# Optimization experiments

Measured on AMD Instinct MI355X. Metric: run time of the kernel, lower is better.

## Reference

```python
import jax, jax.numpy as jnp
import numpy as np

# OFDM/MIMO constants from the source module
N = 512        # subcarriers
N_R = 2        # rx antennas
N_T = 2        # tx antennas
M_BITS = 4     # bits per QAM symbol (16-QAM)
CP = 7         # cyclic prefix = IsiDuration - 1
NO = 1e-5
EBNO_DB = 10.0
BATCH = 4096

# unit-average-power 16-QAM: per-axis levels, index = re_idx + 4*im_idx, bits LSB-first
LEV = jnp.asarray(np.array([-3.0, -1.0, 1.0, 3.0], np.float32) / np.sqrt(10.0))
_idx = np.arange(2 ** M_BITS)
CONST = jnp.asarray(((np.array([-3., -1., 1., 3.]) / np.sqrt(10.))[_idx % 4]
                     + 1j * (np.array([-3., -1., 1., 3.]) / np.sqrt(10.))[_idx // 4]).astype(np.complex64))


def setup_inputs() -> dict:
    key = jax.random.key(0)
    k1, k2, k3 = jax.random.split(key, 3)
    y_data_nld = jax.random.normal(k1, (BATCH, N_R, N + CP, 2), jnp.float32)
    y_ls = jax.random.normal(k2, (BATCH, N_R, N + CP, 2), jnp.float32)
    x_ls_idx = jax.random.randint(k3, (BATCH, N_T, N), 0, 2 ** M_BITS)
    return {"y_data_nld": y_data_nld, "y_ls": y_ls, "x_ls_idx": x_ls_idx}


def _c(x):
    return jax.lax.complex(x[..., 0], x[..., 1])


def _interp_c(xq, xp, fp):
    # fp: [M, P] complex -> [M, N] complex, linear interp per row (np.interp semantics)
    return jax.vmap(lambda fr, fi: jnp.interp(xq, xp, fr) + 1j * jnp.interp(xq, xp, fi))(fp.real, fp.imag)


def _forward(y_data_nld, y_ls, x_ls_idx):
    B = y_data_nld.shape[0]
    pi = 10.0 ** (EBNO_DB / 10.0) * NO * N          # = 0.0512
    sqrt_pi = jnp.sqrt(jnp.float32(pi))

    # strip CP, FFT, normalize (1/N * fft)
    Y = jnp.fft.fft(_c(y_data_nld)[..., CP:], axis=-1) / N            # [B, N_r, N]
    Y_l = jnp.fft.fft(_c(y_ls)[..., CP:], axis=-1) / (N * sqrt_pi)     # [B, N_r, N]

    x_ls = CONST[x_ls_idx]                                             # [B, N_t, N] pilots

    # comb-type LS estimates + linear interpolation to all N subcarriers
    xq = jnp.arange(N, dtype=jnp.float32)
    H_t = []
    for t in range(N_T):
        comb = jnp.arange(t, N, N_T)                                   # pilot subcarriers for tx t
        pil = Y_l[:, :, comb] / x_ls[:, None, t, comb]                 # [B, N_r, N/N_t]
        if t == 0:
            xp = jnp.concatenate([comb, jnp.array([N - 1])]).astype(jnp.float32)
            fp = jnp.concatenate([pil, pil[..., -1:]], axis=-1)
        else:
            xp = jnp.concatenate([jnp.array([0]), comb]).astype(jnp.float32)
            fp = jnp.concatenate([pil[..., :1], pil], axis=-1)
        P = fp.shape[-1]
        H_t.append(_interp_c(xq, xp, fp.reshape(B * N_R, P)).reshape(B, N_R, N))
    Hm = jnp.stack(H_t, axis=-1)                                       # [B, N_r, N, N_t]
    Hm = jnp.transpose(Hm, (0, 2, 1, 3))                               # [B, N, N_r, N_t]

    # per-subcarrier 2x2 linear solve: X_hat = H^{-1} Y / sqrt(pi)
    X_hat = jnp.linalg.solve(Hm, jnp.transpose(Y, (0, 2, 1))[..., None])[..., 0] / sqrt_pi  # [B, N, N_t]
    x_hat_ri = jnp.stack([X_hat.real, X_hat.imag], axis=-1)            # [B, N, N_t, 2]

    # nearest-QAM demap (square 16-QAM: per-axis argmin == joint argmin), bits LSB-first
    vre = jnp.argmin((X_hat.real[..., None] - LEV) ** 2, axis=-1)      # [B, N, N_t]
    vim = jnp.argmin((X_hat.imag[..., None] - LEV) ** 2, axis=-1)
    qidx = vre + 4 * vim
    bits = (qidx[..., None] >> jnp.arange(M_BITS)) & 1                 # [B, N, N_t, m]
    b_hat = jnp.transpose(bits, (0, 2, 1, 3)).reshape(B, N_T, N * M_BITS).astype(jnp.float32)
    return x_hat_ri, b_hat


def reference(y_data_nld, y_ls, x_ls_idx):
    return _forward(y_data_nld, y_ls, x_ls_idx)
```

## Files before the change

kernel.cpp:

```cpp
#include <hip/hip_runtime.h>
#include <math.h>

namespace {

constexpr int NSC  = 512;
constexpr int CP   = 7;
constexpr int NTOT = 519;

__device__ __forceinline__ int padidx(int x) { return x + (x >> 5); }

struct cf { float x, y; };
__device__ __forceinline__ cf cadd(cf a, cf b) { return {a.x + b.x, a.y + b.y}; }
__device__ __forceinline__ cf csub(cf a, cf b) { return {a.x - b.x, a.y - b.y}; }
__device__ __forceinline__ cf cmul(cf a, cf b) { return {a.x*b.x - a.y*b.y, a.x*b.y + a.y*b.x}; }
__device__ __forceinline__ cf mni(cf a) { return {a.y, -a.x}; }

__device__ __forceinline__ void fft8(cf a[8]) {
    const float s = 0.70710678118654752f;
    cf b0 = a[0], b1 = a[4], b2 = a[2], b3 = a[6];
    cf b4 = a[1], b5 = a[5], b6 = a[3], b7 = a[7];
    cf c0 = cadd(b0, b1), c1 = csub(b0, b1);
    cf c2 = cadd(b2, b3), c3 = csub(b2, b3);
    cf c4 = cadd(b4, b5), c5 = csub(b4, b5);
    cf c6 = cadd(b6, b7), c7 = csub(b6, b7);
    cf d0 = cadd(c0, c2), d2 = csub(c0, c2);
    cf d1 = cadd(c1, mni(c3)), d3 = csub(c1, mni(c3));
    cf d4 = cadd(c4, c6), d6 = csub(c4, c6);
    cf d5 = cadd(c5, mni(c7)), d7 = csub(c5, mni(c7));
    cf e5 = { s * (d5.x + d5.y), s * (d5.y - d5.x) };
    cf e6 = mni(d6);
    cf e7 = { s * (d7.y - d7.x), -s * (d7.x + d7.y) };
    a[0] = cadd(d0, d4); a[4] = csub(d0, d4);
    a[1] = cadd(d1, e5); a[5] = csub(d1, e5);
    a[2] = cadd(d2, e6); a[6] = csub(d2, e6);
    a[3] = cadd(d3, e7); a[7] = csub(d3, e7);
}

struct cd { double x, y; };
__device__ __forceinline__ cd cmuld(cd a, cd b) { return {a.x*b.x - a.y*b.y, a.x*b.y + a.y*b.x}; }
__device__ __forceinline__ cd csubd(cd a, cd b) { return {a.x - b.x, a.y - b.y}; }
__device__ __forceinline__ cd cdivd(cd a, cd b) {
    double d = b.x*b.x + b.y*b.y;
    return {(a.x*b.x + a.y*b.y) / d, (a.y*b.x - a.x*b.y) / d};
}

__global__ __launch_bounds__(256) void ofdm_mimo_kernel(
    const float* __restrict__ y_data,
    const float* __restrict__ y_ls,
    const int*   __restrict__ x_idx,
    float*       __restrict__ out,
    int B)
{
    __shared__ float sr[4][528];
    __shared__ float si[4][528];
    __shared__ float2 pil[2][2][NSC / 2];

    const int b   = blockIdx.x;
    const int tid = threadIdx.x;
    const int q   = tid >> 6;
    const int t   = tid & 63;

    const float data_scale = 1.0f / 512.0f;
    const float ls_scale   = (float)(1.0 / (512.0 * 0.22627416997969522));

    const int r = q & 1;
    const float* srcp = (q < 2) ? y_data : y_ls;
    const float sc = (q < 2) ? data_scale : ls_scale;
    const float2* xin = (const float2*)(srcp + ((size_t)(b * 2 + r) * NTOT + CP) * 2);

    cf a[8];
    #pragma unroll
    for (int n2 = 0; n2 < 8; ++n2) {
        float2 v = xin[t + 64 * n2];
        a[n2] = { v.x * sc, v.y * sc };
    }
    fft8(a);

    {
        const int n1 = t >> 3;
        const float w64 = -6.2831853071795864769f / 64.0f;
        #pragma unroll
        for (int k0 = 1; k0 < 8; ++k0) {
            float sn, cs;
            __sincosf(w64 * (float)(n1 * k0), &sn, &cs);
            a[k0] = cmul(a[k0], {cs, sn});
        }
    }
    #pragma unroll
    for (int k0 = 0; k0 < 8; ++k0) {
        int p = padidx(t * 8 + k0);
        sr[q][p] = a[k0].x;
        si[q][p] = a[k0].y;
    }
    __syncthreads();

    #pragma unroll
    for (int n1 = 0; n1 < 8; ++n1) {
        int p = padidx(n1 * 64 + (t & 7) * 8 + (t >> 3));
        a[n1] = { sr[q][p], si[q][p] };
    }
    __syncthreads();
    fft8(a);

    {
        const int n0 = t & 7, k0 = t >> 3;
        const float w512 = -6.2831853071795864769f / 512.0f;
        #pragma unroll
        for (int k1 = 0; k1 < 8; ++k1) {
            float sn, cs;
            __sincosf(w512 * (float)(n0 * (k0 + 8 * k1)), &sn, &cs);
            a[k1] = cmul(a[k1], {cs, sn});
        }
    }
    #pragma unroll
    for (int k1 = 0; k1 < 8; ++k1) {
        int p = padidx((t & 7) * 64 + (t >> 3) * 8 + k1);
        sr[q][p] = a[k1].x;
        si[q][p] = a[k1].y;
    }
    __syncthreads();

    #pragma unroll
    for (int n0 = 0; n0 < 8; ++n0) {
        int p = padidx(n0 * 64 + (t >> 3) * 8 + (t & 7));
        a[n0] = { sr[q][p], si[q][p] };
    }
    __syncthreads();
    fft8(a);

    #pragma unroll
    for (int k2 = 0; k2 < 8; ++k2) {
        int p = padidx((t >> 3) + 8 * (t & 7) + 64 * k2);
        sr[q][p] = a[k2].x;
        si[q][p] = a[k2].y;
    }
    __syncthreads();

    const float lev[4] = {-0.9486832980505138f, -0.31622776601683794f,
                           0.31622776601683794f, 0.9486832980505138f};
    #pragma unroll
    for (int pi = tid; pi < 1024; pi += 256) {
        int tt = pi >> 9;
        int rr = (pi >> 8) & 1;
        int k  = pi & 255;
        int comb = tt + 2 * k;
        int pc = padidx(comb);
        int idx = x_idx[((size_t)b * 2 + tt) * NSC + comb];
        float xr = lev[idx & 3];
        float xi = lev[(idx >> 2) & 3];
        float ylr = sr[2 + rr][pc];
        float yli = si[2 + rr][pc];
        float inv = 1.0f / (xr * xr + xi * xi);
        pil[tt][rr][k] = make_float2((ylr * xr + yli * xi) * inv,
                                     (yli * xr - ylr * xi) * inv);
    }
    __syncthreads();

    #pragma unroll
    for (int ni = 0; ni < 2; ++ni) {
        const int n = tid + 256 * ni;
        cd H[2][2];
        #pragma unroll
        for (int rr = 0; rr < 2; ++rr) {
            float2 h0;
            if ((n & 1) == 0) {
                h0 = pil[0][rr][n >> 1];
            } else if (n == NSC - 1) {
                h0 = pil[0][rr][255];
            } else {
                float2 aa = pil[0][rr][n >> 1];
                float2 cc = pil[0][rr][(n >> 1) + 1];
                h0 = make_float2(0.5f * (aa.x + cc.x), 0.5f * (aa.y + cc.y));
            }
            float2 h1;
            if (n & 1) {
                h1 = pil[1][rr][n >> 1];
            } else if (n == 0) {
                h1 = pil[1][rr][0];
            } else {
                float2 aa = pil[1][rr][(n >> 1) - 1];
                float2 cc = pil[1][rr][n >> 1];
                h1 = make_float2(0.5f * (aa.x + cc.x), 0.5f * (aa.y + cc.y));
            }
            H[rr][0] = {(double)h0.x, (double)h0.y};
            H[rr][1] = {(double)h1.x, (double)h1.y};
        }
        int pn = padidx(n);
        cd Y0 = {(double)sr[0][pn], (double)si[0][pn]};
        cd Y1 = {(double)sr[1][pn], (double)si[1][pn]};

        cd det = csubd(cmuld(H[0][0], H[1][1]), cmuld(H[0][1], H[1][0]));
        cd X0  = cdivd(csubd(cmuld(H[1][1], Y0), cmuld(H[0][1], Y1)), det);
        cd X1  = cdivd(csubd(cmuld(H[0][0], Y1), cmuld(H[1][0], Y0)), det);
        const double inv_sqrt_pi = 1.0 / 0.22627416997969522;
        X0.x *= inv_sqrt_pi; X0.y *= inv_sqrt_pi;
        X1.x *= inv_sqrt_pi; X1.y *= inv_sqrt_pi;

        float4* xo = (float4*)(out + (size_t)b * 2048 + (size_t)n * 4);
        *xo = make_float4((float)X0.x, (float)X0.y, (float)X1.x, (float)X1.y);

        const double bnd = 0.6324555320336759;
        auto qi = [&](double v) -> int {
            return (v <= -bnd) ? 0 : (v <= 0.0) ? 1 : (v <= bnd) ? 2 : 3;
        };
        int vre0 = qi(X0.x), vim0 = qi(X0.y);
        int vre1 = qi(X1.x), vim1 = qi(X1.y);

        size_t bbase = (size_t)B * 2048;
        float4* b0 = (float4*)(out + bbase + ((size_t)b * 2 + 0) * 2048 + (size_t)n * 4);
        *b0 = make_float4((float)(vre0 & 1), (float)((vre0 >> 1) & 1),
                          (float)(vim0 & 1), (float)((vim0 >> 1) & 1));
        float4* b1 = (float4*)(out + bbase + ((size_t)b * 2 + 1) * 2048 + (size_t)n * 4);
        *b1 = make_float4((float)(vre1 & 1), (float)((vre1 >> 1) & 1),
                          (float)(vim1 & 1), (float)((vim1 >> 1) & 1));
    }
}

}

extern "C" void kernel_launch(void* const* d_in, const int* in_sizes, int n_in,
                              void* d_out, int out_size, void* d_ws, size_t ws_size,
                              hipStream_t stream) {
    const float* y_data = (const float*)d_in[0];
    const float* y_ls   = (const float*)d_in[1];
    const int*   x_idx  = (const int*)d_in[2];
    float* out = (float*)d_out;

    int B = in_sizes[0] / (2 * NTOT * 2);
    ofdm_mimo_kernel<<<B, 256, 0, stream>>>(y_data, y_ls, x_idx, out, B);
}
```

Measured before the change: 40.88 us.

## Replace block barriers with wave barriers, reuse LDS for pilots, fold scale

Each wave owns one FFT row, so the block-wide syncthreads inside the FFT stages become wave barriers. The separate pilot LDS array is removed and pilot estimates are written back into the LS rows of the existing buffers, which needs an extra barrier and staging through registers. The 1/sqrt(pi) output scaling is folded into the data FFT scale, and launch bounds ask for 8 blocks per CU. Less LDS and fewer barriers should raise occupancy and cut sync stalls, but the changed scale ordering could move results slightly near decision boundaries.

```diff
diff --git a/kernel.cpp b/kernel.cpp
--- a/kernel.cpp
+++ b/kernel.cpp
@@ -44,7 +44,7 @@
     return {(a.x*b.x + a.y*b.y) / d, (a.y*b.x - a.x*b.y) / d};
 }
 
-__global__ __launch_bounds__(256) void ofdm_mimo_kernel(
+__global__ __launch_bounds__(256, 8) void ofdm_mimo_kernel(
     const float* __restrict__ y_data,
     const float* __restrict__ y_ls,
     const int*   __restrict__ x_idx,
@@ -53,19 +53,16 @@
 {
     __shared__ float sr[4][528];
     __shared__ float si[4][528];
-    __shared__ float2 pil[2][2][NSC / 2];
 
     const int b   = blockIdx.x;
     const int tid = threadIdx.x;
     const int q   = tid >> 6;
     const int t   = tid & 63;
 
-    const float data_scale = 1.0f / 512.0f;
-    const float ls_scale   = (float)(1.0 / (512.0 * 0.22627416997969522));
+    const float sc = (float)(1.0 / (512.0 * 0.22627416997969522));
 
     const int r = q & 1;
     const float* srcp = (q < 2) ? y_data : y_ls;
-    const float sc = (q < 2) ? data_scale : ls_scale;
     const float2* xin = (const float2*)(srcp + ((size_t)(b * 2 + r) * NTOT + CP) * 2);
 
     cf a[8];
@@ -92,14 +89,14 @@
         sr[q][p] = a[k0].x;
         si[q][p] = a[k0].y;
     }
-    __syncthreads();
+    __builtin_amdgcn_wave_barrier();
 
     #pragma unroll
     for (int n1 = 0; n1 < 8; ++n1) {
         int p = padidx(n1 * 64 + (t & 7) * 8 + (t >> 3));
         a[n1] = { sr[q][p], si[q][p] };
     }
-    __syncthreads();
+    __builtin_amdgcn_wave_barrier();
     fft8(a);
 
     {
@@ -118,14 +115,14 @@
         sr[q][p] = a[k1].x;
         si[q][p] = a[k1].y;
     }
-    __syncthreads();
+    __builtin_amdgcn_wave_barrier();
 
     #pragma unroll
     for (int n0 = 0; n0 < 8; ++n0) {
         int p = padidx(n0 * 64 + (t >> 3) * 8 + (t & 7));
         a[n0] = { sr[q][p], si[q][p] };
     }
-    __syncthreads();
+    __builtin_amdgcn_wave_barrier();
     fft8(a);
 
     #pragma unroll
@@ -138,21 +135,38 @@
 
     const float lev[4] = {-0.9486832980505138f, -0.31622776601683794f,
                            0.31622776601683794f, 0.9486832980505138f};
-    #pragma unroll
-    for (int pi = tid; pi < 1024; pi += 256) {
-        int tt = pi >> 9;
-        int rr = (pi >> 8) & 1;
-        int k  = pi & 255;
+    float pr[2][2], pim[2][2];
+    #pragma unroll
+    for (int j = 0; j < 2; ++j) {
+        int u  = tid + 256 * j;
+        int tt = u >> 8;
+        int k  = u & 255;
         int comb = tt + 2 * k;
-        int pc = padidx(comb);
-        int idx = x_idx[((size_t)b * 2 + tt) * NSC + comb];
+        int idx = x_idx[((size_t)(b * 2 + tt)) * NSC + comb];
         float xr = lev[idx & 3];
         float xi = lev[(idx >> 2) & 3];
-        float ylr = sr[2 + rr][pc];
-        float yli = si[2 + rr][pc];
         float inv = 1.0f / (xr * xr + xi * xi);
-        pil[tt][rr][k] = make_float2((ylr * xr + yli * xi) * inv,
-                                     (yli * xr - ylr * xi) * inv);
+        int pc = padidx(comb);
+        #pragma unroll
+        for (int rr = 0; rr < 2; ++rr) {
+            float ylr = sr[2 + rr][pc];
+            float yli = si[2 + rr][pc];
+            pr[j][rr]  = (ylr * xr + yli * xi) * inv;
+            pim[j][rr] = (yli * xr - ylr * xi) * inv;
+        }
+    }
+    __syncthreads();
+    #pragma unroll
+    for (int j = 0; j < 2; ++j) {
+        int u  = tid + 256 * j;
+        int tt = u >> 8;
+        int k  = u & 255;
+        #pragma unroll
+        for (int rr = 0; rr < 2; ++rr) {
+            int p = padidx(rr * 256 + k);
+            sr[2 + tt][p] = pr[j][rr];
+            si[2 + tt][p] = pim[j][rr];
+        }
     }
     __syncthreads();
 
@@ -162,25 +176,30 @@
         cd H[2][2];
         #pragma unroll
         for (int rr = 0; rr < 2; ++rr) {
-            float2 h0;
+            float2 h0, h1;
             if ((n & 1) == 0) {
-                h0 = pil[0][rr][n >> 1];
+                int p = padidx(rr * 256 + (n >> 1));
+                h0 = make_float2(sr[2][p], si[2][p]);
             } else if (n == NSC - 1) {
-                h0 = pil[0][rr][255];
+                int p = padidx(rr * 256 + 255);
+                h0 = make_float2(sr[2][p], si[2][p]);
             } else {
-                float2 aa = pil[0][rr][n >> 1];
-                float2 cc = pil[0][rr][(n >> 1) + 1];
-                h0 = make_float2(0.5f * (aa.x + cc.x), 0.5f * (aa.y + cc.y));
+                int pa = padidx(rr * 256 + (n >> 1));
+                int pb = padidx(rr * 256 + (n >> 1) + 1);
+                h0 = make_float2(0.5f * (sr[2][pa] + sr[2][pb]),
+                                 0.5f * (si[2][pa] + si[2][pb]));
             }
-            float2 h1;
             if (n & 1) {
-                h1 = pil[1][rr][n >> 1];
+                int p = padidx(rr * 256 + (n >> 1));
+                h1 = make_float2(sr[3][p], si[3][p]);
             } else if (n == 0) {
-                h1 = pil[1][rr][0];
+                int p = padidx(rr * 256 + 0);
+                h1 = make_float2(sr[3][p], si[3][p]);
             } else {
-                float2 aa = pil[1][rr][(n >> 1) - 1];
-                float2 cc = pil[1][rr][n >> 1];
-                h1 = make_float2(0.5f * (aa.x + cc.x), 0.5f * (aa.y + cc.y));
+                int pa = padidx(rr * 256 + (n >> 1) - 1);
+                int pb = padidx(rr * 256 + (n >> 1));
+                h1 = make_float2(0.5f * (sr[3][pa] + sr[3][pb]),
+                                 0.5f * (si[3][pa] + si[3][pb]));
             }
             H[rr][0] = {(double)h0.x, (double)h0.y};
             H[rr][1] = {(double)h1.x, (double)h1.y};
@@ -192,9 +211,6 @@
         cd det = csubd(cmuld(H[0][0], H[1][1]), cmuld(H[0][1], H[1][0]));
         cd X0  = cdivd(csubd(cmuld(H[1][1], Y0), cmuld(H[0][1], Y1)), det);
         cd X1  = cdivd(csubd(cmuld(H[0][0], Y1), cmuld(H[1][0], Y0)), det);
-        const double inv_sqrt_pi = 1.0 / 0.22627416997969522;
-        X0.x *= inv_sqrt_pi; X0.y *= inv_sqrt_pi;
-        X1.x *= inv_sqrt_pi; X1.y *= inv_sqrt_pi;
 
         float4* xo = (float4*)(out + (size_t)b * 2048 + (size_t)n * 4);
         *xo = make_float4((float)X0.x, (float)X0.y, (float)X1.x, (float)X1.y);
```

Result: faster. 39.32 us (-3.8%).
